# Performance work log

Measured on AMD Instinct MI355X. Metric: run time of the kernel, lower is better.

Reference implementation:

```python
import jax, jax.numpy as jnp
import numpy as np

VOCAB = 1_000_000
DIM = 128
BATCH = 4096
WINDOW = 5
NEG = 5
LMAX = 4
NROWS = BATCH * 2 * WINDOW  # 40960


def setup_inputs() -> dict:
    key = jax.random.key(0)
    ks = jax.random.split(key, 8)
    initrange = 0.5 / DIM
    u_table = jax.random.uniform(ks[0], (VOCAB, DIM), jnp.float32, -initrange, initrange)
    # original inits v to zeros; use small uniform for a non-degenerate baseline
    v_table = jax.random.uniform(ks[1], (VOCAB, DIM), jnp.float32, -initrange, initrange)
    pos_u_idx = jax.random.randint(ks[2], (NROWS, LMAX), 0, VOCAB)
    pos_v_idx = jax.random.randint(ks[3], (NROWS, LMAX), 0, VOCAB)
    neg_v_idx = jax.random.randint(ks[4], (NROWS * NEG, LMAX), 0, VOCAB)
    pos_u_len = jax.random.randint(ks[5], (NROWS,), 1, LMAX + 1)
    pos_v_len = jax.random.randint(ks[6], (NROWS,), 1, LMAX + 1)
    neg_v_len = jax.random.randint(ks[7], (NROWS * NEG,), 1, LMAX + 1)
    return {
        "u_table": u_table, "v_table": v_table,
        "pos_u_idx": pos_u_idx, "pos_u_len": pos_u_len,
        "pos_v_idx": pos_v_idx, "pos_v_len": pos_v_len,
        "neg_v_idx": neg_v_idx, "neg_v_len": neg_v_len,
        "batch_size": BATCH,
    }


def _bag_mean(table, idx, lengths):
    # ragged embedding-bag mean: gather [rows, L, D], mask padded slots, mean over valid
    emb = table[idx]  # [rows, L, D]
    mask = (jnp.arange(idx.shape[1])[None, :] < lengths[:, None]).astype(emb.dtype)
    summed = jnp.einsum('rld,rl->rd', emb, mask)
    return summed / lengths[:, None].astype(emb.dtype)


def reference(u_table, v_table, pos_u_idx, pos_u_len, pos_v_idx, pos_v_len,
              neg_v_idx, neg_v_len, batch_size):
    embed_u = _bag_mean(u_table, pos_u_idx, pos_u_len)        # [N, D]
    embed_v = _bag_mean(v_table, pos_v_idx, pos_v_len)        # [N, D]
    neg_v = _bag_mean(v_table, neg_v_idx, neg_v_len)          # [N*K, D]
    neg_v = neg_v.reshape(embed_u.shape[0], NEG, DIM)         # [N, K, D]

    score = jnp.sum(embed_u * embed_v, axis=1)                # [N]
    log_target = jax.nn.log_sigmoid(score)
    neg_score = jnp.einsum('nkd,nd->nk', neg_v, embed_u)      # [N, K]
    sum_log_sampled = jnp.sum(jax.nn.log_sigmoid(-neg_score), axis=1)
    loss = log_target + sum_log_sampled
    return -jnp.sum(loss) / batch_size
```

## Files before the change

### kernel.cpp

```cpp
#include <hip/hip_runtime.h>
#include <math.h>


constexpr int NROWS = 40960;
constexpr int NEG   = 5;
constexpr int LMAX  = 4;
constexpr int D4    = 32;
constexpr int MAIN_BLOCKS = NROWS * 32 / 256;

__device__ __forceinline__ float log_sigmoidf(float x) {
    return fminf(x, 0.0f) - log1pf(__expf(-fabsf(x)));
}

__global__ __launch_bounds__(256) void skipgram_main(
    const float4* __restrict__ u_table,
    const float4* __restrict__ v_table,
    const int*  __restrict__ pos_u_idx,
    const int*  __restrict__ pos_u_len,
    const int*  __restrict__ pos_v_idx,
    const int*  __restrict__ pos_v_len,
    const int*  __restrict__ neg_v_idx,
    const int*  __restrict__ neg_v_len,
    float* __restrict__ block_sums)
{
    const int tid  = blockIdx.x * 256 + threadIdx.x;
    const int row  = tid >> 5;
    const int lane = threadIdx.x & 31;

    float4 eu = make_float4(0.f, 0.f, 0.f, 0.f);
    {
        const int lu = pos_u_len[row];
        for (int l = 0; l < lu; ++l) {
            const int idx = pos_u_idx[row * LMAX + l];
            const float4 t = u_table[(size_t)idx * D4 + lane];
            eu.x += t.x; eu.y += t.y; eu.z += t.z; eu.w += t.w;
        }
        const float inv = 1.0f / (float)lu;
        eu.x *= inv; eu.y *= inv; eu.z *= inv; eu.w *= inv;
    }

    float term;
    {
        float4 ev = make_float4(0.f, 0.f, 0.f, 0.f);
        const int lv = pos_v_len[row];
        for (int l = 0; l < lv; ++l) {
            const int idx = pos_v_idx[row * LMAX + l];
            const float4 t = v_table[(size_t)idx * D4 + lane];
            ev.x += t.x; ev.y += t.y; ev.z += t.z; ev.w += t.w;
        }
        float s = (eu.x*ev.x + eu.y*ev.y + eu.z*ev.z + eu.w*ev.w) / (float)lv;
        #pragma unroll
        for (int off = 16; off > 0; off >>= 1) s += __shfl_xor(s, off);
        term = log_sigmoidf(s);
    }

    #pragma unroll
    for (int k = 0; k < NEG; ++k) {
        const int r  = row * NEG + k;
        const int ln = neg_v_len[r];
        float4 nv = make_float4(0.f, 0.f, 0.f, 0.f);
        for (int l = 0; l < ln; ++l) {
            const int idx = neg_v_idx[r * LMAX + l];
            const float4 t = v_table[(size_t)idx * D4 + lane];
            nv.x += t.x; nv.y += t.y; nv.z += t.z; nv.w += t.w;
        }
        float ns = (eu.x*nv.x + eu.y*nv.y + eu.z*nv.z + eu.w*nv.w) / (float)ln;
        #pragma unroll
        for (int off = 16; off > 0; off >>= 1) ns += __shfl_xor(ns, off);
        term += log_sigmoidf(-ns);
    }

    float wave_sum = term + __shfl_xor(term, 32);

    __shared__ float lds[4];
    if ((threadIdx.x & 63) == 0) lds[threadIdx.x >> 6] = wave_sum;
    __syncthreads();
    if (threadIdx.x == 0)
        block_sums[blockIdx.x] = lds[0] + lds[1] + lds[2] + lds[3];
}

__global__ __launch_bounds__(256) void skipgram_reduce(
    const float* __restrict__ block_sums,
    const int*   __restrict__ batch_size,
    float*       __restrict__ out)
{
    float s = 0.f;
    for (int i = threadIdx.x; i < MAIN_BLOCKS; i += 256) s += block_sums[i];
    #pragma unroll
    for (int off = 32; off > 0; off >>= 1) s += __shfl_xor(s, off);
    __shared__ float lds[4];
    if ((threadIdx.x & 63) == 0) lds[threadIdx.x >> 6] = s;
    __syncthreads();
    if (threadIdx.x == 0) {
        const float tot = lds[0] + lds[1] + lds[2] + lds[3];
        out[0] = -tot / (float)batch_size[0];
    }
}

extern "C" void kernel_launch(void* const* d_in, const int* in_sizes, int n_in,
                              void* d_out, int out_size, void* d_ws, size_t ws_size,
                              hipStream_t stream) {
    const float4* u_table   = (const float4*)d_in[0];
    const float4* v_table   = (const float4*)d_in[1];
    const int*    pos_u_idx = (const int*)d_in[2];
    const int*    pos_u_len = (const int*)d_in[3];
    const int*    pos_v_idx = (const int*)d_in[4];
    const int*    pos_v_len = (const int*)d_in[5];
    const int*    neg_v_idx = (const int*)d_in[6];
    const int*    neg_v_len = (const int*)d_in[7];
    const int*    batch_sz  = (const int*)d_in[8];

    float* block_sums = (float*)d_ws;

    skipgram_main<<<MAIN_BLOCKS, 256, 0, stream>>>(
        u_table, v_table, pos_u_idx, pos_u_len, pos_v_idx, pos_v_len,
        neg_v_idx, neg_v_len, block_sums);

    skipgram_reduce<<<1, 256, 0, stream>>>(block_sums, batch_sz, (float*)d_out);
}
```

Before: 849.7 us.

## Map one wave per row and issue all bag gathers up front

Each 64-lane wavefront now handles one row with float2 lanes instead of two rows per wave with float4. All index and length loads are hoisted and made wave-uniform through readfirstlane. Every u and v gather for the row is issued before any arithmetic, and the six dot-product reductions are interleaved. The aim is more memory-level parallelism on the random row gathers and less serialized loop latency, at the cost of higher register pressure and narrower per-lane loads.

Result: faster. 829.7 us (-2.4%).

```diff
diff --git a/kernel.cpp b/kernel.cpp
--- a/kernel.cpp
+++ b/kernel.cpp
@@ -5,16 +5,18 @@
 constexpr int NROWS = 40960;
 constexpr int NEG   = 5;
 constexpr int LMAX  = 4;
-constexpr int D4    = 32;
-constexpr int MAIN_BLOCKS = NROWS * 32 / 256;
+constexpr int D2    = 64;
+constexpr int MAIN_BLOCKS = NROWS / 4;
 
 __device__ __forceinline__ float log_sigmoidf(float x) {
     return fminf(x, 0.0f) - log1pf(__expf(-fabsf(x)));
 }
 
-__global__ __launch_bounds__(256) void skipgram_main(
-    const float4* __restrict__ u_table,
-    const float4* __restrict__ v_table,
+__device__ __forceinline__ int rfl(int x) { return __builtin_amdgcn_readfirstlane(x); }
+
+__global__ __launch_bounds__(256, 4) void skipgram_main(
+    const float2* __restrict__ u_table,
+    const float2* __restrict__ v_table,
     const int*  __restrict__ pos_u_idx,
     const int*  __restrict__ pos_u_len,
     const int*  __restrict__ pos_v_idx,
@@ -23,57 +25,76 @@
     const int*  __restrict__ neg_v_len,
     float* __restrict__ block_sums)
 {
-    const int tid  = blockIdx.x * 256 + threadIdx.x;
-    const int row  = tid >> 5;
-    const int lane = threadIdx.x & 31;
+    const int lane = threadIdx.x & 63;
+    const int row  = rfl((int)(blockIdx.x * 4 + (threadIdx.x >> 6)));
 
-    float4 eu = make_float4(0.f, 0.f, 0.f, 0.f);
+    const int lu = rfl(pos_u_len[row]);
+    int vlen[6];
+    vlen[0] = rfl(pos_v_len[row]);
     {
-        const int lu = pos_u_len[row];
-        for (int l = 0; l < lu; ++l) {
-            const int idx = pos_u_idx[row * LMAX + l];
-            const float4 t = u_table[(size_t)idx * D4 + lane];
-            eu.x += t.x; eu.y += t.y; eu.z += t.z; eu.w += t.w;
-        }
-        const float inv = 1.0f / (float)lu;
-        eu.x *= inv; eu.y *= inv; eu.z *= inv; eu.w *= inv;
+        const int* nl = neg_v_len + row * NEG;
+        #pragma unroll
+        for (int k = 0; k < NEG; ++k) vlen[k + 1] = rfl(nl[k]);
     }
 
-    float term;
+    int ui[LMAX];
     {
-        float4 ev = make_float4(0.f, 0.f, 0.f, 0.f);
-        const int lv = pos_v_len[row];
-        for (int l = 0; l < lv; ++l) {
-            const int idx = pos_v_idx[row * LMAX + l];
-            const float4 t = v_table[(size_t)idx * D4 + lane];
-            ev.x += t.x; ev.y += t.y; ev.z += t.z; ev.w += t.w;
+        int4 t = *(const int4*)(pos_u_idx + row * LMAX);
+        ui[0] = rfl(t.x); ui[1] = rfl(t.y); ui[2] = rfl(t.z); ui[3] = rfl(t.w);
+    }
+    int vi[6][LMAX];
+    {
+        int4 t = *(const int4*)(pos_v_idx + row * LMAX);
+        vi[0][0] = rfl(t.x); vi[0][1] = rfl(t.y); vi[0][2] = rfl(t.z); vi[0][3] = rfl(t.w);
+        #pragma unroll
+        for (int k = 0; k < NEG; ++k) {
+            int4 n = *(const int4*)(neg_v_idx + (row * NEG + k) * LMAX);
+            vi[k+1][0] = rfl(n.x); vi[k+1][1] = rfl(n.y);
+            vi[k+1][2] = rfl(n.z); vi[k+1][3] = rfl(n.w);
         }
-        float s = (eu.x*ev.x + eu.y*ev.y + eu.z*ev.z + eu.w*ev.w) / (float)lv;
-        #pragma unroll
-        for (int off = 16; off > 0; off >>= 1) s += __shfl_xor(s, off);
-        term = log_sigmoidf(s);
+    }
+
+    const float2 z = make_float2(0.f, 0.f);
+    float2 u0 = u_table[(size_t)ui[0] * D2 + lane];
+    float2 u1 = z, u2 = z, u3 = z;
+    if (lu > 1) u1 = u_table[(size_t)ui[1] * D2 + lane];
+    if (lu > 2) u2 = u_table[(size_t)ui[2] * D2 + lane];
+    if (lu > 3) u3 = u_table[(size_t)ui[3] * D2 + lane];
+
+    float2 t[6][LMAX];
+    #pragma unroll
+    for (int b = 0; b < 6; ++b) {
+        t[b][1] = z; t[b][2] = z; t[b][3] = z;
+        t[b][0] = v_table[(size_t)vi[b][0] * D2 + lane];
+        if (vlen[b] > 1) t[b][1] = v_table[(size_t)vi[b][1] * D2 + lane];
+        if (vlen[b] > 2) t[b][2] = v_table[(size_t)vi[b][2] * D2 + lane];
+        if (vlen[b] > 3) t[b][3] = v_table[(size_t)vi[b][3] * D2 + lane];
+    }
+
+    const float inv_lu = 1.0f / (float)lu;
+    const float eux = (u0.x + u1.x + u2.x + u3.x) * inv_lu;
+    const float euy = (u0.y + u1.y + u2.y + u3.y) * inv_lu;
+
+    float p[6];
+    #pragma unroll
+    for (int b = 0; b < 6; ++b) {
+        const float sx = t[b][0].x + t[b][1].x + t[b][2].x + t[b][3].x;
+        const float sy = t[b][0].y + t[b][1].y + t[b][2].y + t[b][3].y;
+        p[b] = (eux * sx + euy * sy) / (float)vlen[b];
     }
 
     #pragma unroll
-    for (int k = 0; k < NEG; ++k) {
-        const int r  = row * NEG + k;
-        const int ln = neg_v_len[r];
-        float4 nv = make_float4(0.f, 0.f, 0.f, 0.f);
-        for (int l = 0; l < ln; ++l) {
-            const int idx = neg_v_idx[r * LMAX + l];
-            const float4 t = v_table[(size_t)idx * D4 + lane];
-            nv.x += t.x; nv.y += t.y; nv.z += t.z; nv.w += t.w;
-        }
-        float ns = (eu.x*nv.x + eu.y*nv.y + eu.z*nv.z + eu.w*nv.w) / (float)ln;
+    for (int off = 32; off > 0; off >>= 1) {
         #pragma unroll
-        for (int off = 16; off > 0; off >>= 1) ns += __shfl_xor(ns, off);
-        term += log_sigmoidf(-ns);
+        for (int b = 0; b < 6; ++b) p[b] += __shfl_xor(p[b], off);
     }
 
-    float wave_sum = term + __shfl_xor(term, 32);
+    float term = log_sigmoidf(p[0]);
+    #pragma unroll
+    for (int b = 1; b < 6; ++b) term += log_sigmoidf(-p[b]);
 
     __shared__ float lds[4];
-    if ((threadIdx.x & 63) == 0) lds[threadIdx.x >> 6] = wave_sum;
+    if (lane == 0) lds[threadIdx.x >> 6] = term;
     __syncthreads();
     if (threadIdx.x == 0)
         block_sums[blockIdx.x] = lds[0] + lds[1] + lds[2] + lds[3];
@@ -100,8 +121,8 @@
 extern "C" void kernel_launch(void* const* d_in, const int* in_sizes, int n_in,
                               void* d_out, int out_size, void* d_ws, size_t ws_size,
                               hipStream_t stream) {
-    const float4* u_table   = (const float4*)d_in[0];
-    const float4* v_table   = (const float4*)d_in[1];
+    const float2* u_table   = (const float2*)d_in[0];
+    const float2* v_table   = (const float2*)d_in[1];
     const int*    pos_u_idx = (const int*)d_in[2];
     const int*    pos_u_len = (const int*)d_in[3];
     const int*    pos_v_idx = (const int*)d_in[4];
```
